# Kernel tuning notes

Measured on AMD Instinct MI355X. Metric: run time of the kernel, lower is better.

The kernel has to match this reference:

```python
import jax, jax.numpy as jnp
import numpy as np

N, F, C1, H, C2, E = 50000, 256, 32, 8, 16, 800000
NEG_SLOPE = 0.2


def gat_layer(x, src, dst, W, a_src, a_dst, b, heads, out_c, concat):
    n = x.shape[0]
    h = (x @ W).reshape(n, heads, out_c)               # [N,H,C]
    al_src = jnp.sum(h * a_src, axis=-1)               # [N,H]
    al_dst = jnp.sum(h * a_dst, axis=-1)               # [N,H]
    e = jax.nn.leaky_relu(al_src[src] + al_dst[dst], NEG_SLOPE)  # [E,H]
    # segment softmax over incoming edges of each dst node
    m = jax.ops.segment_max(e, dst, num_segments=n)
    e = jnp.exp(e - m[dst])
    denom = jax.ops.segment_sum(e, dst, num_segments=n)
    alpha = e / (denom[dst] + 1e-16)                   # [E,H]
    msg = h[src] * alpha[..., None]                    # [E,H,C]
    out = jax.ops.segment_sum(msg, dst, num_segments=n)
    out = out.reshape(n, heads * out_c) if concat else out.mean(axis=1)
    return out + b


def conv1d(x, w, b):
    # x: [1,C,N], w: [O,I,K], 'same' padding (K=5 -> pad 2)
    pad = (w.shape[-1] - 1) // 2
    y = jax.lax.conv_general_dilated(x, w, (1,), [(pad, pad)],
                                     dimension_numbers=('NCH', 'OIH', 'NCH'))
    return y + b[None, :, None]


def setup_inputs() -> dict:
    key = jax.random.key(0)
    ks = jax.random.split(key, 20)
    s = lambda k, shp, sc: jax.random.normal(k, shp, jnp.float32) * sc
    inp = {
        'x': jax.random.normal(ks[0], (N, F), jnp.float32),
        'edge_index': jax.random.randint(ks[1], (2, E), 0, N, jnp.int32),
        'W1': s(ks[2], (F, H * C1), 0.06),
        'a_src1': s(ks[3], (H, C1), 0.1), 'a_dst1': s(ks[4], (H, C1), 0.1),
        'b1': jnp.zeros((H * C1,), jnp.float32),
        'W2': s(ks[5], (H * C1, C2), 0.06),
        'a_src2': s(ks[6], (1, C2), 0.1), 'a_dst2': s(ks[7], (1, C2), 0.1),
        'b2': jnp.zeros((C2,), jnp.float32),
        'proj_w': s(ks[8], (C2, 1), 0.2), 'proj_b': jnp.zeros((1,), jnp.float32),
        'c1_w': s(ks[9], (C2, C2, 5), 0.1), 'c1_b': jnp.zeros((C2,), jnp.float32),
        'c2_w': s(ks[10], (C2, C2, 5), 0.1), 'c2_b': jnp.zeros((C2,), jnp.float32),
        'lin_w': s(ks[11], (2 * C2, C2), 0.15), 'lin_b': jnp.zeros((C2,), jnp.float32),
    }
    return inp


def reference(x, edge_index, W1, a_src1, a_dst1, b1, W2, a_src2, a_dst2, b2,
              proj_w, proj_b, c1_w, c1_b, c2_w, c2_b, lin_w, lin_b):
    n = x.shape[0]
    loops = jnp.arange(n, dtype=edge_index.dtype)
    src = jnp.concatenate([edge_index[0], loops])  # PyG GATConv adds self-loops
    dst = jnp.concatenate([edge_index[1], loops])

    h = jax.nn.relu(gat_layer(x, src, dst, W1, a_src1, a_dst1, b1, H, C1, True))
    x1 = gat_layer(h, src, dst, W2, a_src2, a_dst2, b2, 1, C2, False)  # [N,C2]

    g = (x1 @ proj_w + proj_b)[:, 0]                  # [N]
    sort_idx = jnp.argsort(g)
    inverse_idx = jnp.argsort(sort_idx)
    sorted_x = g[sort_idx][:, None] * x1[sort_idx]    # [N,C2]
    sx = sorted_x.T[None]                             # [1,C2,N]
    sx = jax.nn.relu(conv1d(sx, c1_w, c1_b))
    sx = conv1d(sx, c2_w, c2_b)
    x2 = sx[0].T[inverse_idx]                         # [N,C2]

    out = jnp.concatenate([x1, x2], axis=1) @ lin_w + lin_b
    return jax.nn.log_softmax(out, axis=1)
```

## Files before the change

kernel.cpp:

```cpp
#include <hip/hip_runtime.h>
#include <math.h>

#define NBUCKET 65536
#define CHUNK_SHIFT 12
#define NCHUNK 16

__device__ __forceinline__ float leakyrelu02(float v) { return v > 0.f ? v : 0.2f * v; }

__global__ __launch_bounds__(256) void k_gemm1(const float* __restrict__ A,
                                               const float* __restrict__ B,
                                               float* __restrict__ C, int M) {
  __shared__ float As[16][68];
  __shared__ float Bs[16][64];
  const int m0 = blockIdx.x * 64;
  const int n0 = blockIdx.y * 64;
  const int tid = threadIdx.x;
  const int tm = tid & 15, tn = tid >> 4;
  float acc[4][4];
#pragma unroll
  for (int i = 0; i < 4; ++i)
#pragma unroll
    for (int j = 0; j < 4; ++j) acc[i][j] = 0.f;

  const int am = tid & 63, ak = (tid >> 6) << 2;
  const int bk = tid >> 4, bn = (tid & 15) << 2;

  for (int k0 = 0; k0 < 256; k0 += 16) {
    float4 av = make_float4(0.f, 0.f, 0.f, 0.f);
    if (m0 + am < M) av = *(const float4*)(A + (size_t)(m0 + am) * 256 + (k0 + ak));
    As[ak + 0][am] = av.x;
    As[ak + 1][am] = av.y;
    As[ak + 2][am] = av.z;
    As[ak + 3][am] = av.w;
    float4 bv = *(const float4*)(B + (size_t)(k0 + bk) * 256 + (n0 + bn));
    *(float4*)&Bs[bk][bn] = bv;
    __syncthreads();
#pragma unroll
    for (int kk = 0; kk < 16; ++kk) {
      float a[4], b[4];
#pragma unroll
      for (int i = 0; i < 4; ++i) a[i] = As[kk][tm * 4 + i];
#pragma unroll
      for (int j = 0; j < 4; ++j) b[j] = Bs[kk][tn * 4 + j];
#pragma unroll
      for (int i = 0; i < 4; ++i)
#pragma unroll
        for (int j = 0; j < 4; ++j) acc[i][j] += a[i] * b[j];
    }
    __syncthreads();
  }
#pragma unroll
  for (int i = 0; i < 4; ++i) {
    int m = m0 + tm * 4 + i;
    if (m < M) {
      float4 o = make_float4(acc[i][0], acc[i][1], acc[i][2], acc[i][3]);
      *(float4*)(C + (size_t)m * 256 + (n0 + tn * 4)) = o;
    }
  }
}

__global__ __launch_bounds__(256) void k_al1(const float* __restrict__ h_lin,
                                             const float* __restrict__ a_src,
                                             const float* __restrict__ a_dst,
                                             float* __restrict__ als,
                                             float* __restrict__ ald, int N) {
  int gid = blockIdx.x * 256 + threadIdx.x;
  int n = gid >> 6;
  int l = threadIdx.x & 63;
  if (n >= N) return;
  float4 h4 = *(const float4*)(h_lin + (size_t)n * 256 + l * 4);
  float4 vs = *(const float4*)(a_src + l * 4);
  float4 vd = *(const float4*)(a_dst + l * 4);
  float ps = h4.x * vs.x + h4.y * vs.y + h4.z * vs.z + h4.w * vs.w;
  float pd = h4.x * vd.x + h4.y * vd.y + h4.z * vd.z + h4.w * vd.w;
  ps += __shfl_xor(ps, 1); pd += __shfl_xor(pd, 1);
  ps += __shfl_xor(ps, 2); pd += __shfl_xor(pd, 2);
  ps += __shfl_xor(ps, 4); pd += __shfl_xor(pd, 4);
  if ((l & 7) == 0) {
    als[(size_t)n * 8 + (l >> 3)] = ps;
    ald[(size_t)n * 8 + (l >> 3)] = pd;
  }
}

__global__ __launch_bounds__(256) void k_hist2(const int* __restrict__ ei,
                                               int* __restrict__ counts2, int E, int N) {
  int e = blockIdx.x * 256 + threadIdx.x;
  if (e >= E + N) return;
  int d, s;
  if (e < E) { d = ei[E + e]; s = ei[e]; }
  else { d = e - E; s = d; }
  atomicAdd(&counts2[d * NCHUNK + (s >> CHUNK_SHIFT)], 1);
}

__global__ __launch_bounds__(256) void k_fold(const int* __restrict__ counts2,
                                              int* __restrict__ counts, int N) {
  int d = blockIdx.x * 256 + threadIdx.x;
  if (d >= N) return;
  int s = 0;
#pragma unroll
  for (int i = 0; i < NCHUNK; i += 4) {
    int4 v = *(const int4*)(counts2 + (size_t)d * NCHUNK + i);
    s += v.x + v.y + v.z + v.w;
  }
  counts[d] = s;
}

__global__ __launch_bounds__(256) void k_expand(const int* __restrict__ offsets,
                                                const int* __restrict__ counts2,
                                                int* __restrict__ cursor2, int N) {
  int d = blockIdx.x * 256 + threadIdx.x;
  if (d >= N) return;
  int run = offsets[d];
#pragma unroll
  for (int i = 0; i < NCHUNK; i += 4) {
    int4 v = *(const int4*)(counts2 + (size_t)d * NCHUNK + i);
    int4 o;
    o.x = run; run += v.x;
    o.y = run; run += v.y;
    o.z = run; run += v.z;
    o.w = run; run += v.w;
    *(int4*)(cursor2 + (size_t)d * NCHUNK + i) = o;
  }
}

__global__ __launch_bounds__(1024) void k_scan(const int* __restrict__ counts,
                                               int* __restrict__ offsets,
                                               int* __restrict__ cursor, int chunk) {
  __shared__ int part[1024];
  const int t = threadIdx.x;
  const int base = t * chunk;
  int ssum = 0;
  for (int i = 0; i < chunk; i += 4) {
    int4 v = *(const int4*)(counts + base + i);
    ssum += v.x + v.y + v.z + v.w;
  }
  part[t] = ssum;
  __syncthreads();
  for (int d = 1; d < 1024; d <<= 1) {
    int v = (t >= d) ? part[t - d] : 0;
    __syncthreads();
    part[t] += v;
    __syncthreads();
  }
  int run = (t == 0) ? 0 : part[t - 1];
  for (int i = 0; i < chunk; i += 4) {
    int4 v = *(const int4*)(counts + base + i);
    int4 o;
    o.x = run; run += v.x;
    o.y = run; run += v.y;
    o.z = run; run += v.z;
    o.w = run; run += v.w;
    *(int4*)(offsets + base + i) = o;
    if (cursor) *(int4*)(cursor + base + i) = o;
  }
  if (t == 1023) offsets[1024 * chunk] = run;
}

__global__ __launch_bounds__(256) void k_scatter_ew(
    const int* __restrict__ ei, const float* __restrict__ als1,
    const float* __restrict__ ald1, int* __restrict__ cursor2,
    int* __restrict__ csr_src, int* __restrict__ csr_dst,
    float* __restrict__ ew, int E, int N) {
  int e = blockIdx.x * 256 + threadIdx.x;
  if (e >= E + N) return;
  int d, s;
  if (e < E) { d = ei[E + e]; s = ei[e]; }
  else { d = e - E; s = d; }
  int pos = atomicAdd(&cursor2[d * NCHUNK + (s >> CHUNK_SHIFT)], 1);
  csr_src[pos] = s;
  csr_dst[pos] = d;
  float4 as0 = *(const float4*)(als1 + (size_t)s * 8);
  float4 as1 = *(const float4*)(als1 + (size_t)s * 8 + 4);
  float4 ad0 = *(const float4*)(ald1 + (size_t)d * 8);
  float4 ad1 = *(const float4*)(ald1 + (size_t)d * 8 + 4);
  float4 w0, w1;
  w0.x = expf(leakyrelu02(as0.x + ad0.x));
  w0.y = expf(leakyrelu02(as0.y + ad0.y));
  w0.z = expf(leakyrelu02(as0.z + ad0.z));
  w0.w = expf(leakyrelu02(as0.w + ad0.w));
  w1.x = expf(leakyrelu02(as1.x + ad1.x));
  w1.y = expf(leakyrelu02(as1.y + ad1.y));
  w1.z = expf(leakyrelu02(as1.z + ad1.z));
  w1.w = expf(leakyrelu02(as1.w + ad1.w));
  *(float4*)(ew + (size_t)pos * 8) = w0;
  *(float4*)(ew + (size_t)pos * 8 + 4) = w1;
}

__global__ __launch_bounds__(256) void k_ew2(const int* __restrict__ csr_src,
                                             const int* __restrict__ csr_dst,
                                             const float* __restrict__ als2,
                                             const float* __restrict__ ald2,
                                             float* __restrict__ ew2, int Etot) {
  int t = blockIdx.x * 256 + threadIdx.x;
  if (t >= Etot) return;
  ew2[t] = expf(leakyrelu02(als2[csr_src[t]] + ald2[csr_dst[t]]));
}

__global__ __launch_bounds__(256) void k_gat1(
    const float* __restrict__ h_lin, const float* __restrict__ ew,
    const float* __restrict__ b1, const int* __restrict__ offsets,
    const int* __restrict__ csr_src, const float* __restrict__ W2,
    const float* __restrict__ a_src2, const float* __restrict__ a_dst2,
    float* __restrict__ h2, float* __restrict__ als2, float* __restrict__ ald2, int N) {
  __shared__ float w2s[4352];
  __shared__ float rowbuf[4][256];
  for (int i = threadIdx.x; i < 4096; i += 256) w2s[(i >> 4) * 17 + (i & 15)] = W2[i];
  __syncthreads();

  const int w = threadIdx.x >> 6;
  const int l = threadIdx.x & 63;
  const int n = blockIdx.x * 4 + w;
  if (n >= N) return;

  const int off = offsets[n];
  const int deg = offsets[n + 1] - off;

  const int h3 = l >> 3;
  const float* hb = h_lin + l * 4;

  float ax = 0.f, ay = 0.f, az = 0.f, aw2 = 0.f, sw = 0.f;
  int e = 0;
  for (; e + 4 <= deg; e += 4) {
    int p = off + e;
    int s0 = csr_src[p + 0];
    int s1 = csr_src[p + 1];
    int s2 = csr_src[p + 2];
    int s3 = csr_src[p + 3];
    float w0 = ew[(size_t)(p + 0) * 8 + h3];
    float w1 = ew[(size_t)(p + 1) * 8 + h3];
    float w2v = ew[(size_t)(p + 2) * 8 + h3];
    float w3 = ew[(size_t)(p + 3) * 8 + h3];
    float4 r0 = *(const float4*)(hb + (size_t)s0 * 256);
    float4 r1 = *(const float4*)(hb + (size_t)s1 * 256);
    float4 r2 = *(const float4*)(hb + (size_t)s2 * 256);
    float4 r3 = *(const float4*)(hb + (size_t)s3 * 256);
    sw += (w0 + w1) + (w2v + w3);
    ax += w0 * r0.x + w1 * r1.x + w2v * r2.x + w3 * r3.x;
    ay += w0 * r0.y + w1 * r1.y + w2v * r2.y + w3 * r3.y;
    az += w0 * r0.z + w1 * r1.z + w2v * r2.z + w3 * r3.z;
    aw2 += w0 * r0.w + w1 * r1.w + w2v * r2.w + w3 * r3.w;
  }
  for (; e < deg; ++e) {
    int p = off + e;
    int s = csr_src[p];
    float ww = ew[(size_t)p * 8 + h3];
    float4 r = *(const float4*)(hb + (size_t)s * 256);
    sw += ww;
    ax += ww * r.x; ay += ww * r.y; az += ww * r.z; aw2 += ww * r.w;
  }
  const float inv = 1.f / (sw + 1e-16f);

  float4 bb = *(const float4*)(b1 + l * 4);
  rowbuf[w][l * 4 + 0] = fmaxf(ax * inv + bb.x, 0.f);
  rowbuf[w][l * 4 + 1] = fmaxf(ay * inv + bb.y, 0.f);
  rowbuf[w][l * 4 + 2] = fmaxf(az * inv + bb.z, 0.f);
  rowbuf[w][l * 4 + 3] = fmaxf(aw2 * inv + bb.w, 0.f);
  asm volatile("s_waitcnt lgkmcnt(0)" ::: "memory");

  const int o = l & 15;
  const int grp = l >> 4;
  float a2 = 0.f;
#pragma unroll 8
  for (int t = 0; t < 64; ++t) {
    int cc = grp * 64 + ((t + grp * 8) & 63);
    a2 += rowbuf[w][cc] * w2s[cc * 17 + o];
  }
  a2 += __shfl_xor(a2, 16);
  a2 += __shfl_xor(a2, 32);

  if (l < 16) {
    h2[(size_t)n * 16 + l] = a2;
    float ps = a2 * a_src2[l];
    float pd = a2 * a_dst2[l];
    ps += __shfl_xor(ps, 1); pd += __shfl_xor(pd, 1);
    ps += __shfl_xor(ps, 2); pd += __shfl_xor(pd, 2);
    ps += __shfl_xor(ps, 4); pd += __shfl_xor(pd, 4);
    ps += __shfl_xor(ps, 8); pd += __shfl_xor(pd, 8);
    if (l == 0) { als2[n] = ps; ald2[n] = pd; }
  }
}

__global__ __launch_bounds__(256) void k_gat2(
    const float* __restrict__ h2, const float* __restrict__ ew2,
    const float* __restrict__ b2, const float* __restrict__ proj_w,
    const float* __restrict__ proj_b, const int* __restrict__ offsets,
    const int* __restrict__ csr_src, float* __restrict__ x1,
    float* __restrict__ g, unsigned long long* __restrict__ keys,
    int* __restrict__ bhist, int N) {
  const int w = threadIdx.x >> 6;
  const int l = threadIdx.x & 63;
  const int n = blockIdx.x * 4 + w;
  if (n >= N) return;
  const int off = offsets[n];
  const int deg = offsets[n + 1] - off;
  const int slot = l >> 4;
  const int c = l & 15;

  float acc = 0.f, sw = 0.f;
  int e0 = 0;
  for (; e0 + 8 <= deg; e0 += 8) {
    int pA = off + e0 + slot;
    int pB = off + e0 + 4 + slot;
    int sA = csr_src[pA];
    int sB = csr_src[pB];
    float wA = ew2[pA];
    float wB = ew2[pB];
    float hA = h2[(size_t)sA * 16 + c];
    float hB = h2[(size_t)sB * 16 + c];
    sw += wA + wB;
    acc += wA * hA + wB * hB;
  }
  for (; e0 < deg; e0 += 4) {
    int e = e0 + slot;
    if (e < deg) {
      int p = off + e;
      int s = csr_src[p];
      float v = ew2[p];
      sw += v;
      acc += v * h2[(size_t)s * 16 + c];
    }
  }
  acc += __shfl_xor(acc, 16); sw += __shfl_xor(sw, 16);
  acc += __shfl_xor(acc, 32); sw += __shfl_xor(sw, 32);
  float x1v = acc / (sw + 1e-16f) + b2[c];

  float pg = x1v * proj_w[c];
  pg += __shfl_xor(pg, 1);
  pg += __shfl_xor(pg, 2);
  pg += __shfl_xor(pg, 4);
  pg += __shfl_xor(pg, 8);
  if (l < 16) x1[(size_t)n * 16 + l] = x1v;
  if (l == 0) {
    float gv = pg + proj_b[0];
    g[n] = gv;
    unsigned u = __float_as_uint(gv);
    u = (u & 0x80000000u) ? ~u : (u | 0x80000000u);
    keys[n] = (((unsigned long long)u) << 32) | (unsigned)n;
    atomicAdd(&bhist[u >> 16], 1);
  }
}

__global__ __launch_bounds__(256) void k_bscatter(const unsigned long long* __restrict__ keys,
                                                  int* __restrict__ cursor,
                                                  unsigned long long* __restrict__ bkeys, int N) {
  int n = blockIdx.x * 256 + threadIdx.x;
  if (n >= N) return;
  unsigned long long k = keys[n];
  int b = (int)(k >> 48);
  int pos = atomicAdd(&cursor[b], 1);
  bkeys[pos] = k;
}

__global__ __launch_bounds__(256) void k_brank(const unsigned long long* __restrict__ bkeys,
                                               const int* __restrict__ boffs,
                                               const float* __restrict__ g,
                                               const float* __restrict__ x1,
                                               int* __restrict__ rank,
                                               float* __restrict__ sortedv, int N) {
  int pos = blockIdx.x * 256 + threadIdx.x;
  if (pos >= N) return;
  unsigned long long k = bkeys[pos];
  int b = (int)(k >> 48);
  int lo = boffs[b], hi = boffs[b + 1];
  int r = lo;
  for (int j = lo; j < hi; ++j) r += (bkeys[j] < k) ? 1 : 0;
  int idx = (int)(unsigned)(k & 0xffffffffull);
  rank[idx] = r;
  float gv = g[idx];
#pragma unroll
  for (int c = 0; c < 16; c += 4) {
    float4 v = *(const float4*)(x1 + (size_t)idx * 16 + c);
    float4 o = make_float4(gv * v.x, gv * v.y, gv * v.z, gv * v.w);
    *(float4*)(sortedv + (size_t)r * 16 + c) = o;
  }
}

__global__ __launch_bounds__(256) void k_conv(const float* __restrict__ in,
                                              const float* __restrict__ wgt,
                                              const float* __restrict__ bias,
                                              float* __restrict__ out, int N, int relu) {
  __shared__ float s[260][17];
  __shared__ float ws[1280];
  __shared__ float bs[16];
  const int p0 = blockIdx.x * 256;
  for (int i = threadIdx.x; i < 1280; i += 256) ws[i] = wgt[i];
  if (threadIdx.x < 16) bs[threadIdx.x] = bias[threadIdx.x];
  for (int idx = threadIdx.x; idx < 260 * 16; idx += 256) {
    int lp = idx >> 4, c = idx & 15;
    int gp = p0 - 2 + lp;
    s[lp][c] = (gp >= 0 && gp < N) ? in[(size_t)gp * 16 + c] : 0.f;
  }
  __syncthreads();
  const int p = p0 + threadIdx.x;
  if (p >= N) return;
  float acc[16];
#pragma unroll
  for (int o = 0; o < 16; ++o) acc[o] = bs[o];
  for (int k = 0; k < 5; ++k) {
    for (int c = 0; c < 16; ++c) {
      float xv = s[threadIdx.x + k][c];
#pragma unroll
      for (int o = 0; o < 16; ++o) acc[o] += ws[(o * 16 + c) * 5 + k] * xv;
    }
  }
#pragma unroll
  for (int o = 0; o < 16; ++o) {
    float v = acc[o];
    if (relu) v = fmaxf(v, 0.f);
    out[(size_t)p * 16 + o] = v;
  }
}

__global__ __launch_bounds__(256) void k_final(
    const float* __restrict__ x1, const float* __restrict__ c2out,
    const int* __restrict__ rank, const float* __restrict__ lin_w,
    const float* __restrict__ lin_b, float* __restrict__ out, int N) {
  __shared__ float lw[512];
  __shared__ float lb[16];
  for (int i = threadIdx.x; i < 512; i += 256) lw[i] = lin_w[i];
  if (threadIdx.x < 16) lb[threadIdx.x] = lin_b[threadIdx.x];
  __syncthreads();
  const int n = blockIdx.x * 256 + threadIdx.x;
  if (n >= N) return;
  float xa[16], xb[16];
  const int r = rank[n];
#pragma unroll
  for (int c = 0; c < 16; c += 4) {
    float4 va = *(const float4*)(x1 + (size_t)n * 16 + c);
    float4 vb = *(const float4*)(c2out + (size_t)r * 16 + c);
    xa[c] = va.x; xa[c + 1] = va.y; xa[c + 2] = va.z; xa[c + 3] = va.w;
    xb[c] = vb.x; xb[c + 1] = vb.y; xb[c + 2] = vb.z; xb[c + 3] = vb.w;
  }
  float z[16];
#pragma unroll
  for (int o = 0; o < 16; ++o) z[o] = lb[o];
#pragma unroll
  for (int c = 0; c < 16; ++c) {
    float va = xa[c], vb = xb[c];
#pragma unroll
    for (int o = 0; o < 16; ++o) z[o] += va * lw[c * 16 + o] + vb * lw[(16 + c) * 16 + o];
  }
  float m = z[0];
#pragma unroll
  for (int o = 1; o < 16; ++o) m = fmaxf(m, z[o]);
  float ssum = 0.f;
#pragma unroll
  for (int o = 0; o < 16; ++o) ssum += expf(z[o] - m);
  float lse = m + logf(ssum);
#pragma unroll
  for (int o = 0; o < 16; ++o) out[(size_t)n * 16 + o] = z[o] - lse;
}

extern "C" void kernel_launch(void* const* d_in, const int* in_sizes, int n_in,
                              void* d_out, int out_size, void* d_ws, size_t ws_size,
                              hipStream_t stream) {
  const float* x = (const float*)d_in[0];
  const int* ei = (const int*)d_in[1];
  const float* W1 = (const float*)d_in[2];
  const float* a_src1 = (const float*)d_in[3];
  const float* a_dst1 = (const float*)d_in[4];
  const float* b1 = (const float*)d_in[5];
  const float* W2 = (const float*)d_in[6];
  const float* a_src2 = (const float*)d_in[7];
  const float* a_dst2 = (const float*)d_in[8];
  const float* b2 = (const float*)d_in[9];
  const float* proj_w = (const float*)d_in[10];
  const float* proj_b = (const float*)d_in[11];
  const float* c1_w = (const float*)d_in[12];
  const float* c1_b = (const float*)d_in[13];
  const float* c2_w = (const float*)d_in[14];
  const float* c2_b = (const float*)d_in[15];
  const float* lin_w = (const float*)d_in[16];
  const float* lin_b = (const float*)d_in[17];
  float* out = (float*)d_out;

  const int N = in_sizes[0] / 256;
  const int E = in_sizes[1] / 2;
  const int Etot = E + N;

  int chunk = (N + 1023) / 1024;
  chunk = (chunk + 3) & ~3;
  const int Npad = 1024 * chunk;

  char* ws = (char*)d_ws;
  size_t off = 0;
  auto alloc = [&](size_t bytes) -> void* {
    void* p = ws + off;
    off = (off + bytes + 255) & ~(size_t)255;
    return p;
  };
  float* h_lin = (float*)alloc((size_t)N * 256 * 4);
  float* als1 = (float*)alloc((size_t)N * 8 * 4);
  float* ald1 = (float*)alloc((size_t)N * 8 * 4);
  int* counts = (int*)alloc((size_t)Npad * 4);
  int* offsets = (int*)alloc((size_t)(Npad + 1) * 4);
  int* counts2 = (int*)alloc((size_t)N * NCHUNK * 4);
  int* cursor2 = (int*)alloc((size_t)N * NCHUNK * 4);
  int* csr_src = (int*)alloc((size_t)Etot * 4);
  int* csr_dst = (int*)alloc((size_t)Etot * 4);
  float* ew = (float*)alloc((size_t)Etot * 8 * 4);
  float* ew2 = (float*)alloc((size_t)Etot * 4);
  float* h2 = (float*)alloc((size_t)N * 16 * 4);
  float* als2 = (float*)alloc((size_t)N * 4);
  float* ald2 = (float*)alloc((size_t)N * 4);
  float* x1 = (float*)alloc((size_t)N * 16 * 4);
  float* gbuf = (float*)alloc((size_t)N * 4);
  unsigned long long* keys = (unsigned long long*)alloc((size_t)N * 8);
  int* bhist = (int*)alloc((size_t)NBUCKET * 4);
  int* boffs = (int*)alloc((size_t)(NBUCKET + 1) * 4);
  int* bcursor = (int*)alloc((size_t)NBUCKET * 4);
  unsigned long long* bkeys = (unsigned long long*)alloc((size_t)N * 8);
  int* rank = (int*)alloc((size_t)N * 4);
  float* sortedv = (float*)alloc((size_t)N * 16 * 4);
  float* c1out = (float*)alloc((size_t)N * 16 * 4);
  float* c2out = (float*)alloc((size_t)N * 16 * 4);
  if (off > ws_size) return;

  hipMemsetAsync(counts, 0, (size_t)Npad * 4, stream);
  hipMemsetAsync(counts2, 0, (size_t)N * NCHUNK * 4, stream);
  hipMemsetAsync(bhist, 0, (size_t)NBUCKET * 4, stream);

  dim3 gg((N + 63) / 64, 4);
  k_gemm1<<<gg, 256, 0, stream>>>(x, W1, h_lin, N);
  k_al1<<<(N + 3) / 4, 256, 0, stream>>>(h_lin, a_src1, a_dst1, als1, ald1, N);
  k_hist2<<<(Etot + 255) / 256, 256, 0, stream>>>(ei, counts2, E, N);
  k_fold<<<(N + 255) / 256, 256, 0, stream>>>(counts2, counts, N);
  k_scan<<<1, 1024, 0, stream>>>(counts, offsets, nullptr, chunk);
  k_expand<<<(N + 255) / 256, 256, 0, stream>>>(offsets, counts2, cursor2, N);
  k_scatter_ew<<<(Etot + 255) / 256, 256, 0, stream>>>(ei, als1, ald1, cursor2,
                                                       csr_src, csr_dst, ew, E, N);
  k_gat1<<<(N + 3) / 4, 256, 0, stream>>>(h_lin, ew, b1, offsets, csr_src,
                                          W2, a_src2, a_dst2, h2, als2, ald2, N);
  k_ew2<<<(Etot + 255) / 256, 256, 0, stream>>>(csr_src, csr_dst, als2, ald2, ew2, Etot);
  k_gat2<<<(N + 3) / 4, 256, 0, stream>>>(h2, ew2, b2, proj_w, proj_b,
                                          offsets, csr_src, x1, gbuf, keys, bhist, N);
  k_scan<<<1, 1024, 0, stream>>>(bhist, boffs, bcursor, NBUCKET / 1024);
  k_bscatter<<<(N + 255) / 256, 256, 0, stream>>>(keys, bcursor, bkeys, N);
  k_brank<<<(N + 255) / 256, 256, 0, stream>>>(bkeys, boffs, gbuf, x1, rank, sortedv, N);
  k_conv<<<(N + 255) / 256, 256, 0, stream>>>(sortedv, c1_w, c1_b, c1out, N, 1);
  k_conv<<<(N + 255) / 256, 256, 0, stream>>>(c1out, c2_w, c2_b, c2out, N, 0);
  k_final<<<(N + 255) / 256, 256, 0, stream>>>(x1, c2out, rank, lin_w, lin_b, out, N);
}
```

Baseline: 536.4 us.

## Enlarge GEMM tiles, fuse CSR scan kernels, split GAT1 edges across half-waves

Measured after the change: 917.7 us. 71.1% more time.

```diff
diff --git a/kernel.cpp b/kernel.cpp
--- a/kernel.cpp
+++ b/kernel.cpp
@@ -10,51 +10,56 @@
 __global__ __launch_bounds__(256) void k_gemm1(const float* __restrict__ A,
                                                const float* __restrict__ B,
                                                float* __restrict__ C, int M) {
-  __shared__ float As[16][68];
-  __shared__ float Bs[16][64];
-  const int m0 = blockIdx.x * 64;
-  const int n0 = blockIdx.y * 64;
+  __shared__ float As[16][132];
+  __shared__ float Bs[16][132];
+  const int m0 = blockIdx.x * 128;
+  const int n0 = blockIdx.y * 128;
   const int tid = threadIdx.x;
   const int tm = tid & 15, tn = tid >> 4;
-  float acc[4][4];
-#pragma unroll
-  for (int i = 0; i < 4; ++i)
-#pragma unroll
-    for (int j = 0; j < 4; ++j) acc[i][j] = 0.f;
-
-  const int am = tid & 63, ak = (tid >> 6) << 2;
-  const int bk = tid >> 4, bn = (tid & 15) << 2;
+  float acc[8][8];
+#pragma unroll
+  for (int i = 0; i < 8; ++i)
+#pragma unroll
+    for (int j = 0; j < 8; ++j) acc[i][j] = 0.f;
 
   for (int k0 = 0; k0 < 256; k0 += 16) {
-    float4 av = make_float4(0.f, 0.f, 0.f, 0.f);
-    if (m0 + am < M) av = *(const float4*)(A + (size_t)(m0 + am) * 256 + (k0 + ak));
-    As[ak + 0][am] = av.x;
-    As[ak + 1][am] = av.y;
-    As[ak + 2][am] = av.z;
-    As[ak + 3][am] = av.w;
-    float4 bv = *(const float4*)(B + (size_t)(k0 + bk) * 256 + (n0 + bn));
-    *(float4*)&Bs[bk][bn] = bv;
+#pragma unroll
+    for (int i = 0; i < 2; ++i) {
+      int f = tid * 2 + i;
+      int ar = f >> 2, ac = (f & 3) * 4;
+      float4 av = make_float4(0.f, 0.f, 0.f, 0.f);
+      if (m0 + ar < M) av = *(const float4*)(A + (size_t)(m0 + ar) * 256 + k0 + ac);
+      As[ac + 0][ar] = av.x;
+      As[ac + 1][ar] = av.y;
+      As[ac + 2][ar] = av.z;
+      As[ac + 3][ar] = av.w;
+      int br = f >> 5, bc = (f & 31) * 4;
+      float4 bv = *(const float4*)(B + (size_t)(k0 + br) * 256 + n0 + bc);
+      *(float4*)&Bs[br][bc] = bv;
+    }
     __syncthreads();
 #pragma unroll
     for (int kk = 0; kk < 16; ++kk) {
-      float a[4], b[4];
-#pragma unroll
-      for (int i = 0; i < 4; ++i) a[i] = As[kk][tm * 4 + i];
-#pragma unroll
-      for (int j = 0; j < 4; ++j) b[j] = Bs[kk][tn * 4 + j];
-#pragma unroll
-      for (int i = 0; i < 4; ++i)
-#pragma unroll
-        for (int j = 0; j < 4; ++j) acc[i][j] += a[i] * b[j];
+      float a[8], b[8];
+      *(float4*)&a[0] = *(const float4*)&As[kk][tm * 8];
+      *(float4*)&a[4] = *(const float4*)&As[kk][tm * 8 + 4];
+      *(float4*)&b[0] = *(const float4*)&Bs[kk][tn * 8];
+      *(float4*)&b[4] = *(const float4*)&Bs[kk][tn * 8 + 4];
+#pragma unroll
+      for (int i = 0; i < 8; ++i)
+#pragma unroll
+        for (int j = 0; j < 8; ++j) acc[i][j] += a[i] * b[j];
     }
     __syncthreads();
   }
 #pragma unroll
-  for (int i = 0; i < 4; ++i) {
-    int m = m0 + tm * 4 + i;
+  for (int i = 0; i < 8; ++i) {
+    int m = m0 + tm * 8 + i;
     if (m < M) {
-      float4 o = make_float4(acc[i][0], acc[i][1], acc[i][2], acc[i][3]);
-      *(float4*)(C + (size_t)m * 256 + (n0 + tn * 4)) = o;
+      float4 o0 = make_float4(acc[i][0], acc[i][1], acc[i][2], acc[i][3]);
+      float4 o1 = make_float4(acc[i][4], acc[i][5], acc[i][6], acc[i][7]);
+      *(float4*)(C + (size_t)m * 256 + n0 + tn * 8) = o0;
+      *(float4*)(C + (size_t)m * 256 + n0 + tn * 8 + 4) = o1;
     }
   }
 }
@@ -92,34 +97,44 @@
   atomicAdd(&counts2[d * NCHUNK + (s >> CHUNK_SHIFT)], 1);
 }
 
-__global__ __launch_bounds__(256) void k_fold(const int* __restrict__ counts2,
-                                              int* __restrict__ counts, int N) {
-  int d = blockIdx.x * 256 + threadIdx.x;
-  if (d >= N) return;
-  int s = 0;
-#pragma unroll
-  for (int i = 0; i < NCHUNK; i += 4) {
-    int4 v = *(const int4*)(counts2 + (size_t)d * NCHUNK + i);
-    s += v.x + v.y + v.z + v.w;
-  }
-  counts[d] = s;
-}
-
-__global__ __launch_bounds__(256) void k_expand(const int* __restrict__ offsets,
-                                                const int* __restrict__ counts2,
-                                                int* __restrict__ cursor2, int N) {
-  int d = blockIdx.x * 256 + threadIdx.x;
-  if (d >= N) return;
-  int run = offsets[d];
-#pragma unroll
-  for (int i = 0; i < NCHUNK; i += 4) {
-    int4 v = *(const int4*)(counts2 + (size_t)d * NCHUNK + i);
-    int4 o;
-    o.x = run; run += v.x;
-    o.y = run; run += v.y;
-    o.z = run; run += v.z;
-    o.w = run; run += v.w;
-    *(int4*)(cursor2 + (size_t)d * NCHUNK + i) = o;
+__global__ __launch_bounds__(1024) void k_scan_csr(const int* __restrict__ counts2,
+                                                   int* __restrict__ offsets,
+                                                   int* __restrict__ cursor2,
+                                                   int N, int chunk) {
+  __shared__ int part[1024];
+  const int t = threadIdx.x;
+  const int start = t * chunk;
+  const int end = min(start + chunk, N);
+  int ssum = 0;
+  for (int d = start; d < end; ++d) {
+    const int4* c2 = (const int4*)(counts2 + (size_t)d * NCHUNK);
+    int4 v0 = c2[0], v1 = c2[1], v2 = c2[2], v3 = c2[3];
+    ssum += v0.x + v0.y + v0.z + v0.w + v1.x + v1.y + v1.z + v1.w +
+            v2.x + v2.y + v2.z + v2.w + v3.x + v3.y + v3.z + v3.w;
+  }
+  part[t] = ssum;
+  __syncthreads();
+  for (int d = 1; d < 1024; d <<= 1) {
+    int v = (t >= d) ? part[t - d] : 0;
+    __syncthreads();
+    part[t] += v;
+    __syncthreads();
+  }
+  int run = (t == 0) ? 0 : part[t - 1];
+  for (int d = start; d < end; ++d) {
+    offsets[d] = run;
+    const int4* c2 = (const int4*)(counts2 + (size_t)d * NCHUNK);
+#pragma unroll
+    for (int i = 0; i < 4; ++i) {
+      int4 v = c2[i];
+      int4 o;
+      o.x = run; run += v.x;
+      o.y = run; run += v.y;
+      o.z = run; run += v.z;
+      o.w = run; run += v.w;
+      *(int4*)(cursor2 + (size_t)d * NCHUNK + i * 4) = o;
+    }
+    if (d == N - 1) offsets[N] = run;
   }
 }
 
@@ -209,52 +224,79 @@
 
   const int w = threadIdx.x >> 6;
   const int l = threadIdx.x & 63;
+  const int half = l >> 5;
+  const int li = l & 31;
+  const int h3 = li >> 2;
   const int n = blockIdx.x * 4 + w;
   if (n >= N) return;
 
   const int off = offsets[n];
   const int deg = offsets[n + 1] - off;
-
-  const int h3 = l >> 3;
-  const float* hb = h_lin + l * 4;
-
-  float ax = 0.f, ay = 0.f, az = 0.f, aw2 = 0.f, sw = 0.f;
+  const float* hb = h_lin + li * 8;
+
+  float c0 = 0.f, c1 = 0.f, c2 = 0.f, c3 = 0.f, c4 = 0.f, c5 = 0.f, c6 = 0.f, c7 = 0.f;
+  float sw = 0.f;
   int e = 0;
-  for (; e + 4 <= deg; e += 4) {
-    int p = off + e;
-    int s0 = csr_src[p + 0];
-    int s1 = csr_src[p + 1];
-    int s2 = csr_src[p + 2];
-    int s3 = csr_src[p + 3];
-    float w0 = ew[(size_t)(p + 0) * 8 + h3];
-    float w1 = ew[(size_t)(p + 1) * 8 + h3];
-    float w2v = ew[(size_t)(p + 2) * 8 + h3];
-    float w3 = ew[(size_t)(p + 3) * 8 + h3];
-    float4 r0 = *(const float4*)(hb + (size_t)s0 * 256);
-    float4 r1 = *(const float4*)(hb + (size_t)s1 * 256);
-    float4 r2 = *(const float4*)(hb + (size_t)s2 * 256);
-    float4 r3 = *(const float4*)(hb + (size_t)s3 * 256);
+  for (; e + 8 <= deg; e += 8) {
+    const int p0 = off + e + half;
+    int s0 = csr_src[p0];
+    int s1 = csr_src[p0 + 2];
+    int s2 = csr_src[p0 + 4];
+    int s3 = csr_src[p0 + 6];
+    float w0 = ew[(size_t)p0 * 8 + h3];
+    float w1 = ew[(size_t)(p0 + 2) * 8 + h3];
+    float w2v = ew[(size_t)(p0 + 4) * 8 + h3];
+    float w3 = ew[(size_t)(p0 + 6) * 8 + h3];
+    const float* r0p = hb + (size_t)s0 * 256;
+    const float* r1p = hb + (size_t)s1 * 256;
+    const float* r2p = hb + (size_t)s2 * 256;
+    const float* r3p = hb + (size_t)s3 * 256;
+    float4 r0a = *(const float4*)(r0p), r0b = *(const float4*)(r0p + 4);
+    float4 r1a = *(const float4*)(r1p), r1b = *(const float4*)(r1p + 4);
+    float4 r2a = *(const float4*)(r2p), r2b = *(const float4*)(r2p + 4);
+    float4 r3a = *(const float4*)(r3p), r3b = *(const float4*)(r3p + 4);
     sw += (w0 + w1) + (w2v + w3);
-    ax += w0 * r0.x + w1 * r1.x + w2v * r2.x + w3 * r3.x;
-    ay += w0 * r0.y + w1 * r1.y + w2v * r2.y + w3 * r3.y;
-    az += w0 * r0.z + w1 * r1.z + w2v * r2.z + w3 * r3.z;
-    aw2 += w0 * r0.w + w1 * r1.w + w2v * r2.w + w3 * r3.w;
-  }
-  for (; e < deg; ++e) {
-    int p = off + e;
-    int s = csr_src[p];
-    float ww = ew[(size_t)p * 8 + h3];
-    float4 r = *(const float4*)(hb + (size_t)s * 256);
-    sw += ww;
-    ax += ww * r.x; ay += ww * r.y; az += ww * r.z; aw2 += ww * r.w;
-  }
+    c0 += w0 * r0a.x + w1 * r1a.x + w2v * r2a.x + w3 * r3a.x;
+    c1 += w0 * r0a.y + w1 * r1a.y + w2v * r2a.y + w3 * r3a.y;
+    c2 += w0 * r0a.z + w1 * r1a.z + w2v * r2a.z + w3 * r3a.z;
+    c3 += w0 * r0a.w + w1 * r1a.w + w2v * r2a.w + w3 * r3a.w;
+    c4 += w0 * r0b.x + w1 * r1b.x + w2v * r2b.x + w3 * r3b.x;
+    c5 += w0 * r0b.y + w1 * r1b.y + w2v * r2b.y + w3 * r3b.y;
+    c6 += w0 * r0b.z + w1 * r1b.z + w2v * r2b.z + w3 * r3b.z;
+    c7 += w0 * r0b.w + w1 * r1b.w + w2v * r2b.w + w3 * r3b.w;
+  }
+  for (; e < deg; e += 2) {
+    int ee = e + half;
+    if (ee < deg) {
+      int p = off + ee;
+      int s = csr_src[p];
+      float ww = ew[(size_t)p * 8 + h3];
+      const float* rp = hb + (size_t)s * 256;
+      float4 ra = *(const float4*)(rp), rb = *(const float4*)(rp + 4);
+      sw += ww;
+      c0 += ww * ra.x; c1 += ww * ra.y; c2 += ww * ra.z; c3 += ww * ra.w;
+      c4 += ww * rb.x; c5 += ww * rb.y; c6 += ww * rb.z; c7 += ww * rb.w;
+    }
+  }
+  c0 += __shfl_xor(c0, 32); c1 += __shfl_xor(c1, 32);
+  c2 += __shfl_xor(c2, 32); c3 += __shfl_xor(c3, 32);
+  c4 += __shfl_xor(c4, 32); c5 += __shfl_xor(c5, 32);
+  c6 += __shfl_xor(c6, 32); c7 += __shfl_xor(c7, 32);
+  sw += __shfl_xor(sw, 32);
   const float inv = 1.f / (sw + 1e-16f);
 
-  float4 bb = *(const float4*)(b1 + l * 4);
-  rowbuf[w][l * 4 + 0] = fmaxf(ax * inv + bb.x, 0.f);
-  rowbuf[w][l * 4 + 1] = fmaxf(ay * inv + bb.y, 0.f);
-  rowbuf[w][l * 4 + 2] = fmaxf(az * inv + bb.z, 0.f);
-  rowbuf[w][l * 4 + 3] = fmaxf(aw2 * inv + bb.w, 0.f);
+  if (half == 0) {
+    float4 ba = *(const float4*)(b1 + li * 8);
+    float4 bbv = *(const float4*)(b1 + li * 8 + 4);
+    rowbuf[w][li * 8 + 0] = fmaxf(c0 * inv + ba.x, 0.f);
+    rowbuf[w][li * 8 + 1] = fmaxf(c1 * inv + ba.y, 0.f);
+    rowbuf[w][li * 8 + 2] = fmaxf(c2 * inv + ba.z, 0.f);
+    rowbuf[w][li * 8 + 3] = fmaxf(c3 * inv + ba.w, 0.f);
+    rowbuf[w][li * 8 + 4] = fmaxf(c4 * inv + bbv.x, 0.f);
+    rowbuf[w][li * 8 + 5] = fmaxf(c5 * inv + bbv.y, 0.f);
+    rowbuf[w][li * 8 + 6] = fmaxf(c6 * inv + bbv.z, 0.f);
+    rowbuf[w][li * 8 + 7] = fmaxf(c7 * inv + bbv.w, 0.f);
+  }
   asm volatile("s_waitcnt lgkmcnt(0)" ::: "memory");
 
   const int o = l & 15;
@@ -477,10 +519,7 @@
   const int N = in_sizes[0] / 256;
   const int E = in_sizes[1] / 2;
   const int Etot = E + N;
-
-  int chunk = (N + 1023) / 1024;
-  chunk = (chunk + 3) & ~3;
-  const int Npad = 1024 * chunk;
+  const int csr_chunk = (N + 1023) / 1024;
 
   char* ws = (char*)d_ws;
   size_t off = 0;
@@ -492,8 +531,7 @@
   float* h_lin = (float*)alloc((size_t)N * 256 * 4);
   float* als1 = (float*)alloc((size_t)N * 8 * 4);
   float* ald1 = (float*)alloc((size_t)N * 8 * 4);
-  int* counts = (int*)alloc((size_t)Npad * 4);
-  int* offsets = (int*)alloc((size_t)(Npad + 1) * 4);
+  int* offsets = (int*)alloc((size_t)(N + 1) * 4);
   int* counts2 = (int*)alloc((size_t)N * NCHUNK * 4);
   int* cursor2 = (int*)alloc((size_t)N * NCHUNK * 4);
   int* csr_src = (int*)alloc((size_t)Etot * 4);
@@ -516,17 +554,14 @@
   float* c2out = (float*)alloc((size_t)N * 16 * 4);
   if (off > ws_size) return;
 
-  hipMemsetAsync(counts, 0, (size_t)Npad * 4, stream);
   hipMemsetAsync(counts2, 0, (size_t)N * NCHUNK * 4, stream);
   hipMemsetAsync(bhist, 0, (size_t)NBUCKET * 4, stream);
 
-  dim3 gg((N + 63) / 64, 4);
+  dim3 gg((N + 127) / 128, 2);
   k_gemm1<<<gg, 256, 0, stream>>>(x, W1, h_lin, N);
   k_al1<<<(N + 3) / 4, 256, 0, stream>>>(h_lin, a_src1, a_dst1, als1, ald1, N);
   k_hist2<<<(Etot + 255) / 256, 256, 0, stream>>>(ei, counts2, E, N);
-  k_fold<<<(N + 255) / 256, 256, 0, stream>>>(counts2, counts, N);
-  k_scan<<<1, 1024, 0, stream>>>(counts, offsets, nullptr, chunk);
-  k_expand<<<(N + 255) / 256, 256, 0, stream>>>(offsets, counts2, cursor2, N);
+  k_scan_csr<<<1, 1024, 0, stream>>>(counts2, offsets, cursor2, N, csr_chunk);
   k_scatter_ew<<<(Etot + 255) / 256, 256, 0, stream>>>(ei, als1, ald1, cursor2,
                                                        csr_src, csr_dst, ew, E, N);
   k_gat1<<<(N + 3) / 4, 256, 0, stream>>>(h_lin, ew, b1, offsets, csr_src,
```
